# Optimization experiments

Measured on AMD Instinct MI355X. Metric: run time of the kernel, lower is better.

The kernel has to match this reference:

```python
import jax, jax.numpy as jnp
import numpy as np

B, S, D, H = 2, 4096, 512, 8
HD = D // H

def setup_inputs() -> dict:
    key = jax.random.key(0)
    ks = jax.random.split(key, 9)
    s = 1.0 / np.sqrt(D)
    inp = {"x": jax.random.normal(ks[0], (B, S, D), dtype=jnp.float32)}
    names = ["Wq", "Wk", "Wv", "Wo"]
    for i, n in enumerate(names):
        inp[n] = jax.random.uniform(ks[1 + 2 * i], (D, D), jnp.float32, -s, s)
        inp["b" + n[1]] = jax.random.uniform(ks[2 + 2 * i], (D,), jnp.float32, -s, s)
    return inp


def reference(x, Wq, bq, Wk, bk, Wv, bv, Wo, bo):
    # projections (torch Linear: x @ W.T + b)
    def proj(W, b):
        return (x @ W.T + b).reshape(B, S, H, HD).transpose(0, 2, 1, 3)  # [B,H,S,HD]
    q = proj(Wq, bq)
    k = proj(Wk, bk)
    v = proj(Wv, bv)
    scores = jnp.einsum("bhqd,bhkd->bhqk", q, k) / np.sqrt(HD).astype(np.float32)
    attn = jax.nn.softmax(scores, axis=-1)
    out = jnp.einsum("bhqk,bhkd->bhqd", attn, v)
    out = out.transpose(0, 2, 1, 3).reshape(B, S, D)
    return out @ Wo.T + bo
```

## Files before the change

kernel.cpp:

```cpp
#include <hip/hip_runtime.h>
#include <hip/hip_bf16.h>

#define DEV __device__ __forceinline__

typedef float f32x4 __attribute__((ext_vector_type(4)));
typedef float f32x16 __attribute__((ext_vector_type(16)));
typedef __bf16 bf16x8 __attribute__((ext_vector_type(8)));
typedef unsigned short u16;
typedef unsigned short u16x8 __attribute__((ext_vector_type(8)));

DEV u16 f2bf(float f) {
    __bf16 h = (__bf16)f;
    return __builtin_bit_cast(u16, h);
}
DEV float bf2f(u16 u) {
    __bf16 h = __builtin_bit_cast(__bf16, u);
    return (float)h;
}

DEV f32x4 mfma16(bf16x8 a, bf16x8 b, f32x4 c) {
    return __builtin_amdgcn_mfma_f32_16x16x32_bf16(a, b, c, 0, 0, 0);
}
DEV f32x16 mfma32(bf16x8 a, bf16x8 b, f32x16 c) {
    return __builtin_amdgcn_mfma_f32_32x32x16_bf16(a, b, c, 0, 0, 0);
}

DEV unsigned cvtpk(float lo, float hi) {
    unsigned r;
    asm("v_cvt_pk_bf16_f32 %0, %1, %2" : "=v"(r) : "v"(lo), "v"(hi));
    return r;
}
DEV void pswap(unsigned& a, unsigned& b) {
    asm volatile("v_permlane32_swap_b32 %0, %1" : "+v"(a), "+v"(b));
}

DEV int kidx(int row, int col) { return row * 64 + (col ^ ((row & 7) << 3)); }
DEV int xidx(int row, int col) { return row * 32 + (col ^ ((row & 3) << 3)); }

__global__ __launch_bounds__(256) void cvt_kernel(
    const float* __restrict__ wq, const float* __restrict__ wk,
    const float* __restrict__ wv, const float* __restrict__ wo,
    u16* __restrict__ wb)
{
    size_t e0 = ((size_t)blockIdx.x * 256 + threadIdx.x) * 8;
    int seg = (int)(e0 >> 18);
    const float* src = (seg == 0) ? wq : (seg == 1) ? wk : (seg == 2) ? wv : wo;
    u16* dst = wb + (size_t)seg * 262144;
    size_t off = e0 & 262143;
    f32x4 a = *(const f32x4*)(src + off);
    f32x4 b = *(const f32x4*)(src + off + 4);
    u16x8 o;
    #pragma unroll
    for (int i = 0; i < 4; ++i) { o[i] = f2bf(a[i]); o[i + 4] = f2bf(b[i]); }
    *(u16x8*)(dst + off) = o;
}

__global__ __launch_bounds__(256) void proj_qkv_kernel(
    const float* __restrict__ x, const u16* __restrict__ wb,
    const float* __restrict__ bq, const float* __restrict__ bk, const float* __restrict__ bv,
    u16* __restrict__ qo, u16* __restrict__ ko, u16* __restrict__ vo)
{
    __shared__ u16 Xs[128 * 32], Wsh[128 * 32];
    const int tid = threadIdx.x;
    const int m0 = blockIdx.x * 128, n0 = blockIdx.y * 128, z = blockIdx.z;
    const u16* W = wb + (size_t)z * 262144;
    const float* bias = (z == 0) ? bq : (z == 1) ? bk : bv;

    const int lane = tid & 63, wv = tid >> 6;
    const int g = lane >> 4, c = lane & 15;
    const int wr = wv >> 1, wcl = wv & 1;
    const int srow = tid >> 1, scol = (tid & 1) * 16;

    f32x4 acc[4][4] = {};

    for (int k0 = 0; k0 < 512; k0 += 32) {
        const float* xp = x + (size_t)(m0 + srow) * 512 + k0 + scol;
        const u16* wp = W + (size_t)(n0 + srow) * 512 + k0 + scol;
        f32x4 xa = *(const f32x4*)xp,       xb2 = *(const f32x4*)(xp + 4);
        f32x4 xc = *(const f32x4*)(xp + 8), xd  = *(const f32x4*)(xp + 12);
        uint4 wa = *(const uint4*)wp, wa2 = *(const uint4*)(wp + 8);
        __syncthreads();
        u16x8 px0, px1;
        #pragma unroll
        for (int j = 0; j < 4; ++j) {
            px0[j] = f2bf(xa[j]); px0[j + 4] = f2bf(xb2[j]);
            px1[j] = f2bf(xc[j]); px1[j + 4] = f2bf(xd[j]);
        }
        *(u16x8*)&Xs[xidx(srow, scol)]      = px0;
        *(u16x8*)&Xs[xidx(srow, scol + 8)]  = px1;
        *(uint4*)&Wsh[xidx(srow, scol)]     = wa;
        *(uint4*)&Wsh[xidx(srow, scol + 8)] = wa2;
        __syncthreads();

        bf16x8 af[4], bfr[4];
        #pragma unroll
        for (int mt = 0; mt < 4; ++mt)
            af[mt] = *(const bf16x8*)&Xs[xidx(wr * 64 + mt * 16 + c, g * 8)];
        #pragma unroll
        for (int nt = 0; nt < 4; ++nt)
            bfr[nt] = *(const bf16x8*)&Wsh[xidx(wcl * 64 + nt * 16 + c, g * 8)];

        if (z < 2) {
            #pragma unroll
            for (int mt = 0; mt < 4; ++mt)
                #pragma unroll
                for (int nt = 0; nt < 4; ++nt)
                    acc[mt][nt] = mfma16(af[mt], bfr[nt], acc[mt][nt]);
        } else {
            #pragma unroll
            for (int mt = 0; mt < 4; ++mt)
                #pragma unroll
                for (int nt = 0; nt < 4; ++nt)
                    acc[mt][nt] = mfma16(bfr[nt], af[mt], acc[mt][nt]);
        }
    }

    if (z < 2) {
        const float scale = (z == 0) ? 0.18033688011112042f : 1.0f;
        u16* outp = (z == 0) ? qo : ko;
        float bn[4];
        #pragma unroll
        for (int nt = 0; nt < 4; ++nt) bn[nt] = bias[n0 + wcl * 64 + nt * 16 + c];
        #pragma unroll
        for (int mt = 0; mt < 4; ++mt)
            #pragma unroll
            for (int r = 0; r < 4; ++r) {
                int mg = m0 + wr * 64 + mt * 16 + g * 4 + r;
                int b = mg >> 12, s = mg & 4095;
                #pragma unroll
                for (int nt = 0; nt < 4; ++nt) {
                    int ng = n0 + wcl * 64 + nt * 16 + c;
                    int h = ng >> 6, d = ng & 63;
                    outp[((size_t)(b * 8 + h) * 4096 + s) * 64 + d] =
                        f2bf((acc[mt][nt][r] + bn[nt]) * scale);
                }
            }
    } else {
        #pragma unroll
        for (int nt = 0; nt < 4; ++nt)
            #pragma unroll
            for (int r = 0; r < 4; ++r) {
                int ng = n0 + wcl * 64 + nt * 16 + g * 4 + r;
                int h = ng >> 6, d = ng & 63;
                float bnr = bias[ng];
                #pragma unroll
                for (int mt = 0; mt < 4; ++mt) {
                    int mg = m0 + wr * 64 + mt * 16 + c;
                    int b = mg >> 12, s = mg & 4095;
                    vo[((size_t)(b * 8 + h) * 64 + d) * 4096 + s] =
                        f2bf(acc[mt][nt][r] + bnr);
                }
            }
    }
}

__global__ __launch_bounds__(256, 4) void flash_attn_kernel(
    const u16* __restrict__ Q, const u16* __restrict__ K,
    const u16* __restrict__ Vt, u16* __restrict__ Opart, float* __restrict__ lbuf)
{
    __shared__ u16 Ks[2][64 * 64];
    __shared__ u16 Vs[2][64 * 64];

    const int tid = threadIdx.x;
    const int bh = blockIdx.y;
    const int q0 = blockIdx.x * 128;
    const int half = blockIdx.z;
    const int kvbase = half * 2048;
    const int lane = tid & 63, wv = tid >> 6;
    const int l31 = lane & 31, hi = lane >> 5;

    const u16* Qb = Q  + (size_t)bh * (4096 * 64);
    const u16* Kb = K  + (size_t)bh * (4096 * 64);
    const u16* Vb = Vt + (size_t)bh * (64 * 4096);

    const int qrow = q0 + wv * 32 + l31;
    bf16x8 qf[4];
    #pragma unroll
    for (int ds = 0; ds < 4; ++ds)
        qf[ds] = *(const bf16x8*)(Qb + (size_t)qrow * 64 + ds * 16 + hi * 8);

    f32x16 oA[2] = {};
    float l_ = 0.f;

    const int sr = tid >> 3, sc8 = (tid & 7) * 8;
    const u16* kp0 = Kb + (size_t)(kvbase + sr) * 64 + sc8;
    const u16* vp0 = Vb + (size_t)sr * 4096 + kvbase + sc8;

    uint4 rk0 = *(const uint4*)(kp0);
    uint4 rk1 = *(const uint4*)(kp0 + 32 * 64);
    uint4 rv0 = *(const uint4*)(vp0);
    uint4 rv1 = *(const uint4*)(vp0 + 32 * 4096);

    for (int t = 0; t < 32; ++t) {
        const int p = t & 1;
        *(uint4*)&Ks[p][kidx(sr, sc8)]      = rk0;
        *(uint4*)&Ks[p][kidx(sr + 32, sc8)] = rk1;
        *(uint4*)&Vs[p][kidx(sr, sc8)]      = rv0;
        *(uint4*)&Vs[p][kidx(sr + 32, sc8)] = rv1;
        if (t < 31) {
            const int kv1 = (t + 1) * 64;
            rk0 = *(const uint4*)(kp0 + (size_t)kv1 * 64);
            rk1 = *(const uint4*)(kp0 + (size_t)(kv1 + 32) * 64);
            rv0 = *(const uint4*)(vp0 + kv1);
            rv1 = *(const uint4*)(vp0 + 32 * 4096 + kv1);
        }
        __syncthreads();

        #pragma unroll
        for (int ct = 0; ct < 2; ++ct) {
            f32x16 sA = {};
            __builtin_amdgcn_s_setprio(1);
            #pragma unroll
            for (int ds = 0; ds < 4; ++ds) {
                bf16x8 kf = *(const bf16x8*)&Ks[p][kidx(ct * 32 + l31, ds * 16 + hi * 8)];
                sA = mfma32(kf, qf[ds], sA);
            }
            __builtin_amdgcn_s_setprio(0);

            float pv[16];
            #pragma unroll
            for (int r = 0; r < 16; ++r)
                pv[r] = __builtin_amdgcn_exp2f(sA[r]);
            #pragma unroll
            for (int r = 0; r < 16; r += 4)
                l_ += (pv[r] + pv[r + 1]) + (pv[r + 2] + pv[r + 3]);

            unsigned a0 = cvtpk(pv[0],  pv[1]),  a1 = cvtpk(pv[2],  pv[3]);
            unsigned b0 = cvtpk(pv[4],  pv[5]),  b1 = cvtpk(pv[6],  pv[7]);
            pswap(a0, b0); pswap(a1, b1);
            uint4 w0; w0.x = a0; w0.y = a1; w0.z = b0; w0.w = b1;
            bf16x8 pfa = __builtin_bit_cast(bf16x8, w0);
            unsigned c0 = cvtpk(pv[8],  pv[9]),  c1 = cvtpk(pv[10], pv[11]);
            unsigned d0 = cvtpk(pv[12], pv[13]), d1 = cvtpk(pv[14], pv[15]);
            pswap(c0, d0); pswap(c1, d1);
            uint4 w1; w1.x = c0; w1.y = c1; w1.z = d0; w1.w = d1;
            bf16x8 pfb = __builtin_bit_cast(bf16x8, w1);

            __builtin_amdgcn_s_setprio(1);
            #pragma unroll
            for (int hf = 0; hf < 2; ++hf) {
                const int ks = 2 * ct + hf;
                const bf16x8 pfx = hf ? pfb : pfa;
                bf16x8 vf0 = *(const bf16x8*)&Vs[p][kidx(l31,      ks * 16 + hi * 8)];
                bf16x8 vf1 = *(const bf16x8*)&Vs[p][kidx(32 + l31, ks * 16 + hi * 8)];
                oA[0] = mfma32(vf0, pfx, oA[0]);
                oA[1] = mfma32(vf1, pfx, oA[1]);
            }
            __builtin_amdgcn_s_setprio(0);
        }
    }

    float l_full = l_ + __shfl_xor(l_, 32);
    if (hi == 0)
        lbuf[(size_t)(half * 16 + bh) * 4096 + qrow] = l_full;

    const int b = bh >> 3, h = bh & 7;
    u16* Ob = Opart + (size_t)half * 4194304 +
              ((size_t)(b * 4096 + qrow)) * 512 + h * 64;
    #pragma unroll
    for (int dt = 0; dt < 2; ++dt) {
        const f32x16 oa = dt ? oA[1] : oA[0];
        #pragma unroll
        for (int qd = 0; qd < 4; ++qd) {
            unsigned w0 = cvtpk(oa[qd * 4 + 0], oa[qd * 4 + 1]);
            unsigned w1 = cvtpk(oa[qd * 4 + 2], oa[qd * 4 + 3]);
            uint2 st; st.x = w0; st.y = w1;
            *(uint2*)(Ob + dt * 32 + qd * 8 + hi * 4) = st;
        }
    }
}

__global__ __launch_bounds__(256) void combine_kernel(
    const u16* __restrict__ Opart, const float* __restrict__ lbuf,
    u16* __restrict__ obuf)
{
    const size_t idx8 = ((size_t)blockIdx.x * 256 + threadIdx.x) * 8;
    const int m = (int)(idx8 >> 9);
    const int hd = (int)(idx8 & 511);
    const int b = m >> 12, s = m & 4095, h = hd >> 6;
    const int bh = b * 8 + h;
    const float la = lbuf[(size_t)bh * 4096 + s];
    const float lb = lbuf[(size_t)(16 + bh) * 4096 + s];
    const float inv = 1.0f / (la + lb);
    u16x8 a = *(const u16x8*)(Opart + idx8);
    u16x8 c = *(const u16x8*)(Opart + 4194304 + idx8);
    u16x8 o;
    #pragma unroll
    for (int i = 0; i < 8; ++i)
        o[i] = f2bf((bf2f(a[i]) + bf2f(c[i])) * inv);
    *(u16x8*)(obuf + idx8) = o;
}

__global__ __launch_bounds__(256) void out_proj_kernel(
    const u16* __restrict__ Ob, const u16* __restrict__ Wob,
    const float* __restrict__ bo, float* __restrict__ out)
{
    __shared__ u16 Xs[128 * 32], Wsh[128 * 32];
    const int tid = threadIdx.x;
    const int m0 = blockIdx.x * 128, n0 = blockIdx.y * 128;

    const int lane = tid & 63, wv = tid >> 6;
    const int g = lane >> 4, c = lane & 15;
    const int wr = wv >> 1, wcl = wv & 1;
    const int srow = tid >> 1, scol = (tid & 1) * 16;

    f32x4 acc[4][4] = {};

    for (int k0 = 0; k0 < 512; k0 += 32) {
        const u16* xp = Ob  + (size_t)(m0 + srow) * 512 + k0 + scol;
        const u16* wp = Wob + (size_t)(n0 + srow) * 512 + k0 + scol;
        uint4 xa = *(const uint4*)xp, xa2 = *(const uint4*)(xp + 8);
        uint4 wa = *(const uint4*)wp, wa2 = *(const uint4*)(wp + 8);
        __syncthreads();
        *(uint4*)&Xs[xidx(srow, scol)]      = xa;
        *(uint4*)&Xs[xidx(srow, scol + 8)]  = xa2;
        *(uint4*)&Wsh[xidx(srow, scol)]     = wa;
        *(uint4*)&Wsh[xidx(srow, scol + 8)] = wa2;
        __syncthreads();

        bf16x8 af[4], bfr[4];
        #pragma unroll
        for (int mt = 0; mt < 4; ++mt)
            af[mt] = *(const bf16x8*)&Xs[xidx(wr * 64 + mt * 16 + c, g * 8)];
        #pragma unroll
        for (int nt = 0; nt < 4; ++nt)
            bfr[nt] = *(const bf16x8*)&Wsh[xidx(wcl * 64 + nt * 16 + c, g * 8)];

        #pragma unroll
        for (int mt = 0; mt < 4; ++mt)
            #pragma unroll
            for (int nt = 0; nt < 4; ++nt)
                acc[mt][nt] = mfma16(bfr[nt], af[mt], acc[mt][nt]);
    }

    #pragma unroll
    for (int nt = 0; nt < 4; ++nt) {
        f32x4 bi = *(const f32x4*)&bo[n0 + wcl * 64 + nt * 16 + g * 4];
        #pragma unroll
        for (int mt = 0; mt < 4; ++mt) {
            int m = m0 + wr * 64 + mt * 16 + c;
            f32x4 v;
            #pragma unroll
            for (int r = 0; r < 4; ++r) v[r] = acc[mt][nt][r] + bi[r];
            *(f32x4*)&out[(size_t)m * 512 + n0 + wcl * 64 + nt * 16 + g * 4] = v;
        }
    }
}

extern "C" void kernel_launch(void* const* d_in, const int* in_sizes, int n_in,
                              void* d_out, int out_size, void* d_ws, size_t ws_size,
                              hipStream_t stream) {
    const float* x  = (const float*)d_in[0];
    const float* Wq = (const float*)d_in[1];
    const float* bq = (const float*)d_in[2];
    const float* Wk = (const float*)d_in[3];
    const float* bk = (const float*)d_in[4];
    const float* Wv = (const float*)d_in[5];
    const float* bv = (const float*)d_in[6];
    const float* Wo = (const float*)d_in[7];
    const float* bo = (const float*)d_in[8];
    float* out = (float*)d_out;

    const size_t NQKV = (size_t)2 * 8 * 4096 * 64;
    u16* qw = (u16*)d_ws;
    u16* kw = qw + NQKV;
    u16* vw = kw + NQKV;
    u16* wbuf = vw + NQKV;
    float* lbuf = (float*)(wbuf + 4 * 262144);
    u16* opart = (u16*)d_out;
    u16* obuf = qw;

    cvt_kernel<<<512, 256, 0, stream>>>(Wq, Wk, Wv, Wo, wbuf);
    proj_qkv_kernel<<<dim3(64, 4, 3), 256, 0, stream>>>(x, wbuf, bq, bk, bv, qw, kw, vw);
    flash_attn_kernel<<<dim3(32, 16, 2), 256, 0, stream>>>(qw, kw, vw, opart, lbuf);
    combine_kernel<<<2048, 256, 0, stream>>>(opart, lbuf, obuf);
    out_proj_kernel<<<dim3(64, 4), 256, 0, stream>>>(obuf, wbuf + 3 * 262144, bo, out);
}
```

Measured before the change: 156.8 us.

## Pre-convert x to bf16 once and give each attention wave two query tiles

The conversion kernel now also converts x to bf16 into workspace. The QKV projection reads bf16 x directly instead of converting fp32 x in each of the 12 blocks that share a row tile (three projections times four column tiles). The flash-attention kernel now processes 64 query rows per wave (256 per block), reusing each K fragment and V fragment load across two query tiles. This halves the attention grid and lowers the occupancy bound from 4 to 2, trading fewer LDS reads and less K/V traffic for more registers and less parallelism.

```diff
diff --git a/kernel.cpp b/kernel.cpp
--- a/kernel.cpp
+++ b/kernel.cpp
@@ -38,15 +38,21 @@
 DEV int xidx(int row, int col) { return row * 32 + (col ^ ((row & 3) << 3)); }
 
 __global__ __launch_bounds__(256) void cvt_kernel(
-    const float* __restrict__ wq, const float* __restrict__ wk,
-    const float* __restrict__ wv, const float* __restrict__ wo,
-    u16* __restrict__ wb)
+    const float* __restrict__ x, const float* __restrict__ wq,
+    const float* __restrict__ wk, const float* __restrict__ wv,
+    const float* __restrict__ wo,
+    u16* __restrict__ xb, u16* __restrict__ wb)
 {
     size_t e0 = ((size_t)blockIdx.x * 256 + threadIdx.x) * 8;
-    int seg = (int)(e0 >> 18);
-    const float* src = (seg == 0) ? wq : (seg == 1) ? wk : (seg == 2) ? wv : wo;
-    u16* dst = wb + (size_t)seg * 262144;
-    size_t off = e0 & 262143;
+    const float* src; u16* dst; size_t off;
+    if (e0 < 4194304) { src = x; dst = xb; off = e0; }
+    else {
+        size_t r = e0 - 4194304;
+        int seg = (int)(r >> 18);
+        src = (seg == 0) ? wq : (seg == 1) ? wk : (seg == 2) ? wv : wo;
+        dst = wb + (size_t)seg * 262144;
+        off = r & 262143;
+    }
     f32x4 a = *(const f32x4*)(src + off);
     f32x4 b = *(const f32x4*)(src + off + 4);
     u16x8 o;
@@ -56,7 +62,7 @@
 }
 
 __global__ __launch_bounds__(256) void proj_qkv_kernel(
-    const float* __restrict__ x, const u16* __restrict__ wb,
+    const u16* __restrict__ xb, const u16* __restrict__ wb,
     const float* __restrict__ bq, const float* __restrict__ bk, const float* __restrict__ bv,
     u16* __restrict__ qo, u16* __restrict__ ko, u16* __restrict__ vo)
 {
@@ -74,20 +80,13 @@
     f32x4 acc[4][4] = {};
 
     for (int k0 = 0; k0 < 512; k0 += 32) {
-        const float* xp = x + (size_t)(m0 + srow) * 512 + k0 + scol;
-        const u16* wp = W + (size_t)(n0 + srow) * 512 + k0 + scol;
-        f32x4 xa = *(const f32x4*)xp,       xb2 = *(const f32x4*)(xp + 4);
-        f32x4 xc = *(const f32x4*)(xp + 8), xd  = *(const f32x4*)(xp + 12);
+        const u16* xp = xb + (size_t)(m0 + srow) * 512 + k0 + scol;
+        const u16* wp = W  + (size_t)(n0 + srow) * 512 + k0 + scol;
+        uint4 xa = *(const uint4*)xp, xa2 = *(const uint4*)(xp + 8);
         uint4 wa = *(const uint4*)wp, wa2 = *(const uint4*)(wp + 8);
         __syncthreads();
-        u16x8 px0, px1;
-        #pragma unroll
-        for (int j = 0; j < 4; ++j) {
-            px0[j] = f2bf(xa[j]); px0[j + 4] = f2bf(xb2[j]);
-            px1[j] = f2bf(xc[j]); px1[j + 4] = f2bf(xd[j]);
-        }
-        *(u16x8*)&Xs[xidx(srow, scol)]      = px0;
-        *(u16x8*)&Xs[xidx(srow, scol + 8)]  = px1;
+        *(uint4*)&Xs[xidx(srow, scol)]      = xa;
+        *(uint4*)&Xs[xidx(srow, scol + 8)]  = xa2;
         *(uint4*)&Wsh[xidx(srow, scol)]     = wa;
         *(uint4*)&Wsh[xidx(srow, scol + 8)] = wa2;
         __syncthreads();
@@ -154,7 +153,7 @@
     }
 }
 
-__global__ __launch_bounds__(256, 4) void flash_attn_kernel(
+__global__ __launch_bounds__(256, 2) void flash_attn_kernel(
     const u16* __restrict__ Q, const u16* __restrict__ K,
     const u16* __restrict__ Vt, u16* __restrict__ Opart, float* __restrict__ lbuf)
 {
@@ -163,7 +162,7 @@
 
     const int tid = threadIdx.x;
     const int bh = blockIdx.y;
-    const int q0 = blockIdx.x * 128;
+    const int q0 = blockIdx.x * 256;
     const int half = blockIdx.z;
     const int kvbase = half * 2048;
     const int lane = tid & 63, wv = tid >> 6;
@@ -173,14 +172,16 @@
     const u16* Kb = K  + (size_t)bh * (4096 * 64);
     const u16* Vb = Vt + (size_t)bh * (64 * 4096);
 
-    const int qrow = q0 + wv * 32 + l31;
-    bf16x8 qf[4];
-    #pragma unroll
-    for (int ds = 0; ds < 4; ++ds)
-        qf[ds] = *(const bf16x8*)(Qb + (size_t)qrow * 64 + ds * 16 + hi * 8);
-
-    f32x16 oA[2] = {};
-    float l_ = 0.f;
+    const int qbase = q0 + wv * 64;
+    bf16x8 qf[2][4];
+    #pragma unroll
+    for (int qt = 0; qt < 2; ++qt)
+        #pragma unroll
+        for (int ds = 0; ds < 4; ++ds)
+            qf[qt][ds] = *(const bf16x8*)(Qb + (size_t)(qbase + qt * 32 + l31) * 64 + ds * 16 + hi * 8);
+
+    f32x16 oA[2][2] = {};
+    float l_[2] = {0.f, 0.f};
 
     const int sr = tid >> 3, sc8 = (tid & 7) * 8;
     const u16* kp0 = Kb + (size_t)(kvbase + sr) * 64 + sc8;
@@ -208,64 +209,77 @@
 
         #pragma unroll
         for (int ct = 0; ct < 2; ++ct) {
-            f32x16 sA = {};
-            __builtin_amdgcn_s_setprio(1);
-            #pragma unroll
-            for (int ds = 0; ds < 4; ++ds) {
-                bf16x8 kf = *(const bf16x8*)&Ks[p][kidx(ct * 32 + l31, ds * 16 + hi * 8)];
-                sA = mfma32(kf, qf[ds], sA);
-            }
-            __builtin_amdgcn_s_setprio(0);
-
-            float pv[16];
-            #pragma unroll
-            for (int r = 0; r < 16; ++r)
-                pv[r] = __builtin_amdgcn_exp2f(sA[r]);
-            #pragma unroll
-            for (int r = 0; r < 16; r += 4)
-                l_ += (pv[r] + pv[r + 1]) + (pv[r + 2] + pv[r + 3]);
-
-            unsigned a0 = cvtpk(pv[0],  pv[1]),  a1 = cvtpk(pv[2],  pv[3]);
-            unsigned b0 = cvtpk(pv[4],  pv[5]),  b1 = cvtpk(pv[6],  pv[7]);
-            pswap(a0, b0); pswap(a1, b1);
-            uint4 w0; w0.x = a0; w0.y = a1; w0.z = b0; w0.w = b1;
-            bf16x8 pfa = __builtin_bit_cast(bf16x8, w0);
-            unsigned c0 = cvtpk(pv[8],  pv[9]),  c1 = cvtpk(pv[10], pv[11]);
-            unsigned d0 = cvtpk(pv[12], pv[13]), d1 = cvtpk(pv[14], pv[15]);
-            pswap(c0, d0); pswap(c1, d1);
-            uint4 w1; w1.x = c0; w1.y = c1; w1.z = d0; w1.w = d1;
-            bf16x8 pfb = __builtin_bit_cast(bf16x8, w1);
+            bf16x8 kf[4];
+            #pragma unroll
+            for (int ds = 0; ds < 4; ++ds)
+                kf[ds] = *(const bf16x8*)&Ks[p][kidx(ct * 32 + l31, ds * 16 + hi * 8)];
+
+            bf16x8 pf[2][2];
+            #pragma unroll
+            for (int qt = 0; qt < 2; ++qt) {
+                f32x16 sA = {};
+                __builtin_amdgcn_s_setprio(1);
+                #pragma unroll
+                for (int ds = 0; ds < 4; ++ds)
+                    sA = mfma32(kf[ds], qf[qt][ds], sA);
+                __builtin_amdgcn_s_setprio(0);
+
+                float pv[16];
+                #pragma unroll
+                for (int r = 0; r < 16; ++r)
+                    pv[r] = __builtin_amdgcn_exp2f(sA[r]);
+                #pragma unroll
+                for (int r = 0; r < 16; r += 4)
+                    l_[qt] += (pv[r] + pv[r + 1]) + (pv[r + 2] + pv[r + 3]);
+
+                unsigned a0 = cvtpk(pv[0],  pv[1]),  a1 = cvtpk(pv[2],  pv[3]);
+                unsigned b0 = cvtpk(pv[4],  pv[5]),  b1 = cvtpk(pv[6],  pv[7]);
+                pswap(a0, b0); pswap(a1, b1);
+                uint4 w0; w0.x = a0; w0.y = a1; w0.z = b0; w0.w = b1;
+                pf[qt][0] = __builtin_bit_cast(bf16x8, w0);
+                unsigned c0 = cvtpk(pv[8],  pv[9]),  c1 = cvtpk(pv[10], pv[11]);
+                unsigned d0 = cvtpk(pv[12], pv[13]), d1 = cvtpk(pv[14], pv[15]);
+                pswap(c0, d0); pswap(c1, d1);
+                uint4 w1; w1.x = c0; w1.y = c1; w1.z = d0; w1.w = d1;
+                pf[qt][1] = __builtin_bit_cast(bf16x8, w1);
+            }
 
             __builtin_amdgcn_s_setprio(1);
             #pragma unroll
             for (int hf = 0; hf < 2; ++hf) {
                 const int ks = 2 * ct + hf;
-                const bf16x8 pfx = hf ? pfb : pfa;
                 bf16x8 vf0 = *(const bf16x8*)&Vs[p][kidx(l31,      ks * 16 + hi * 8)];
                 bf16x8 vf1 = *(const bf16x8*)&Vs[p][kidx(32 + l31, ks * 16 + hi * 8)];
-                oA[0] = mfma32(vf0, pfx, oA[0]);
-                oA[1] = mfma32(vf1, pfx, oA[1]);
+                #pragma unroll
+                for (int qt = 0; qt < 2; ++qt) {
+                    oA[qt][0] = mfma32(vf0, pf[qt][hf], oA[qt][0]);
+                    oA[qt][1] = mfma32(vf1, pf[qt][hf], oA[qt][1]);
+                }
             }
             __builtin_amdgcn_s_setprio(0);
         }
     }
 
-    float l_full = l_ + __shfl_xor(l_, 32);
-    if (hi == 0)
-        lbuf[(size_t)(half * 16 + bh) * 4096 + qrow] = l_full;
-
     const int b = bh >> 3, h = bh & 7;
-    u16* Ob = Opart + (size_t)half * 4194304 +
-              ((size_t)(b * 4096 + qrow)) * 512 + h * 64;
-    #pragma unroll
-    for (int dt = 0; dt < 2; ++dt) {
-        const f32x16 oa = dt ? oA[1] : oA[0];
-        #pragma unroll
-        for (int qd = 0; qd < 4; ++qd) {
-            unsigned w0 = cvtpk(oa[qd * 4 + 0], oa[qd * 4 + 1]);
-            unsigned w1 = cvtpk(oa[qd * 4 + 2], oa[qd * 4 + 3]);
-            uint2 st; st.x = w0; st.y = w1;
-            *(uint2*)(Ob + dt * 32 + qd * 8 + hi * 4) = st;
+    #pragma unroll
+    for (int qt = 0; qt < 2; ++qt) {
+        const int qrow = qbase + qt * 32 + l31;
+        float l_full = l_[qt] + __shfl_xor(l_[qt], 32);
+        if (hi == 0)
+            lbuf[(size_t)(half * 16 + bh) * 4096 + qrow] = l_full;
+
+        u16* Ob = Opart + (size_t)half * 4194304 +
+                  ((size_t)(b * 4096 + qrow)) * 512 + h * 64;
+        #pragma unroll
+        for (int dt = 0; dt < 2; ++dt) {
+            const f32x16 oa = oA[qt][dt];
+            #pragma unroll
+            for (int qd = 0; qd < 4; ++qd) {
+                unsigned w0 = cvtpk(oa[qd * 4 + 0], oa[qd * 4 + 1]);
+                unsigned w1 = cvtpk(oa[qd * 4 + 2], oa[qd * 4 + 3]);
+                uint2 st; st.x = w0; st.y = w1;
+                *(uint2*)(Ob + dt * 32 + qd * 8 + hi * 4) = st;
+            }
         }
     }
 }
@@ -367,12 +381,13 @@
     u16* vw = kw + NQKV;
     u16* wbuf = vw + NQKV;
     float* lbuf = (float*)(wbuf + 4 * 262144);
+    u16* xbuf = (u16*)(lbuf + 2 * 16 * 4096);
     u16* opart = (u16*)d_out;
     u16* obuf = qw;
 
-    cvt_kernel<<<512, 256, 0, stream>>>(Wq, Wk, Wv, Wo, wbuf);
-    proj_qkv_kernel<<<dim3(64, 4, 3), 256, 0, stream>>>(x, wbuf, bq, bk, bv, qw, kw, vw);
-    flash_attn_kernel<<<dim3(32, 16, 2), 256, 0, stream>>>(qw, kw, vw, opart, lbuf);
+    cvt_kernel<<<2560, 256, 0, stream>>>(x, Wq, Wk, Wv, Wo, xbuf, wbuf);
+    proj_qkv_kernel<<<dim3(64, 4, 3), 256, 0, stream>>>(xbuf, wbuf, bq, bk, bv, qw, kw, vw);
+    flash_attn_kernel<<<dim3(16, 16, 2), 256, 0, stream>>>(qw, kw, vw, opart, lbuf);
     combine_kernel<<<2048, 256, 0, stream>>>(opart, lbuf, obuf);
     out_proj_kernel<<<dim3(64, 4), 256, 0, stream>>>(obuf, wbuf + 3 * 262144, bo, out);
 }
```

Measured after the change: 140.9 us. 10.1% less time.

## Pre-convert x to bf16 once and compute softmax row sums with MFMA

Applied to the files above, without the earlier changes.

The conversion kernel now also turns the fp32 input x into bf16 in workspace, so the QKV projection reads bf16 x directly instead of re-converting it in each of its 12 N/Z tile blocks. In the attention kernel, the per-lane scalar adds that built the softmax denominator are replaced by an MFMA of the bf16 probability fragments against an all-ones matrix. This moves VALU work onto the matrix cores but sums the rounded bf16 probabilities, which slightly changes the normaliser. The x path adds one extra pass over x in memory in exchange for halving what the projection reads.

```diff
diff --git a/kernel.cpp b/kernel.cpp
--- a/kernel.cpp
+++ b/kernel.cpp
@@ -38,15 +38,21 @@
 DEV int xidx(int row, int col) { return row * 32 + (col ^ ((row & 3) << 3)); }
 
 __global__ __launch_bounds__(256) void cvt_kernel(
-    const float* __restrict__ wq, const float* __restrict__ wk,
-    const float* __restrict__ wv, const float* __restrict__ wo,
-    u16* __restrict__ wb)
+    const float* __restrict__ x, const float* __restrict__ wq,
+    const float* __restrict__ wk, const float* __restrict__ wv,
+    const float* __restrict__ wo,
+    u16* __restrict__ xb, u16* __restrict__ wb)
 {
     size_t e0 = ((size_t)blockIdx.x * 256 + threadIdx.x) * 8;
-    int seg = (int)(e0 >> 18);
-    const float* src = (seg == 0) ? wq : (seg == 1) ? wk : (seg == 2) ? wv : wo;
-    u16* dst = wb + (size_t)seg * 262144;
-    size_t off = e0 & 262143;
+    const float* src; u16* dst; size_t off;
+    if (e0 < 4194304) { src = x; dst = xb; off = e0; }
+    else {
+        size_t r = e0 - 4194304;
+        int seg = (int)(r >> 18);
+        src = (seg == 0) ? wq : (seg == 1) ? wk : (seg == 2) ? wv : wo;
+        dst = wb + (size_t)seg * 262144;
+        off = r & 262143;
+    }
     f32x4 a = *(const f32x4*)(src + off);
     f32x4 b = *(const f32x4*)(src + off + 4);
     u16x8 o;
@@ -56,7 +62,7 @@
 }
 
 __global__ __launch_bounds__(256) void proj_qkv_kernel(
-    const float* __restrict__ x, const u16* __restrict__ wb,
+    const u16* __restrict__ xb, const u16* __restrict__ wb,
     const float* __restrict__ bq, const float* __restrict__ bk, const float* __restrict__ bv,
     u16* __restrict__ qo, u16* __restrict__ ko, u16* __restrict__ vo)
 {
@@ -74,20 +80,13 @@
     f32x4 acc[4][4] = {};
 
     for (int k0 = 0; k0 < 512; k0 += 32) {
-        const float* xp = x + (size_t)(m0 + srow) * 512 + k0 + scol;
-        const u16* wp = W + (size_t)(n0 + srow) * 512 + k0 + scol;
-        f32x4 xa = *(const f32x4*)xp,       xb2 = *(const f32x4*)(xp + 4);
-        f32x4 xc = *(const f32x4*)(xp + 8), xd  = *(const f32x4*)(xp + 12);
+        const u16* xp = xb + (size_t)(m0 + srow) * 512 + k0 + scol;
+        const u16* wp = W  + (size_t)(n0 + srow) * 512 + k0 + scol;
+        uint4 xa = *(const uint4*)xp, xa2 = *(const uint4*)(xp + 8);
         uint4 wa = *(const uint4*)wp, wa2 = *(const uint4*)(wp + 8);
         __syncthreads();
-        u16x8 px0, px1;
-        #pragma unroll
-        for (int j = 0; j < 4; ++j) {
-            px0[j] = f2bf(xa[j]); px0[j + 4] = f2bf(xb2[j]);
-            px1[j] = f2bf(xc[j]); px1[j + 4] = f2bf(xd[j]);
-        }
-        *(u16x8*)&Xs[xidx(srow, scol)]      = px0;
-        *(u16x8*)&Xs[xidx(srow, scol + 8)]  = px1;
+        *(uint4*)&Xs[xidx(srow, scol)]      = xa;
+        *(uint4*)&Xs[xidx(srow, scol + 8)]  = xa2;
         *(uint4*)&Wsh[xidx(srow, scol)]     = wa;
         *(uint4*)&Wsh[xidx(srow, scol + 8)] = wa2;
         __syncthreads();
@@ -173,6 +172,11 @@
     const u16* Kb = K  + (size_t)bh * (4096 * 64);
     const u16* Vb = Vt + (size_t)bh * (64 * 4096);
 
+    u16x8 onesu;
+    #pragma unroll
+    for (int i = 0; i < 8; ++i) onesu[i] = 0x3F80;
+    const bf16x8 ones = __builtin_bit_cast(bf16x8, onesu);
+
     const int qrow = q0 + wv * 32 + l31;
     bf16x8 qf[4];
     #pragma unroll
@@ -180,7 +184,7 @@
         qf[ds] = *(const bf16x8*)(Qb + (size_t)qrow * 64 + ds * 16 + hi * 8);
 
     f32x16 oA[2] = {};
-    float l_ = 0.f;
+    f32x16 oL = {};
 
     const int sr = tid >> 3, sc8 = (tid & 7) * 8;
     const u16* kp0 = Kb + (size_t)(kvbase + sr) * 64 + sc8;
@@ -221,9 +225,6 @@
             #pragma unroll
             for (int r = 0; r < 16; ++r)
                 pv[r] = __builtin_amdgcn_exp2f(sA[r]);
-            #pragma unroll
-            for (int r = 0; r < 16; r += 4)
-                l_ += (pv[r] + pv[r + 1]) + (pv[r + 2] + pv[r + 3]);
 
             unsigned a0 = cvtpk(pv[0],  pv[1]),  a1 = cvtpk(pv[2],  pv[3]);
             unsigned b0 = cvtpk(pv[4],  pv[5]),  b1 = cvtpk(pv[6],  pv[7]);
@@ -237,6 +238,8 @@
             bf16x8 pfb = __builtin_bit_cast(bf16x8, w1);
 
             __builtin_amdgcn_s_setprio(1);
+            oL = mfma32(ones, pfa, oL);
+            oL = mfma32(ones, pfb, oL);
             #pragma unroll
             for (int hf = 0; hf < 2; ++hf) {
                 const int ks = 2 * ct + hf;
@@ -250,9 +253,8 @@
         }
     }
 
-    float l_full = l_ + __shfl_xor(l_, 32);
     if (hi == 0)
-        lbuf[(size_t)(half * 16 + bh) * 4096 + qrow] = l_full;
+        lbuf[(size_t)(half * 16 + bh) * 4096 + qrow] = oL[0];
 
     const int b = bh >> 3, h = bh & 7;
     u16* Ob = Opart + (size_t)half * 4194304 +
@@ -367,11 +369,12 @@
     u16* vw = kw + NQKV;
     u16* wbuf = vw + NQKV;
     float* lbuf = (float*)(wbuf + 4 * 262144);
+    u16* xbuf = (u16*)(lbuf + 2 * 16 * 4096);
     u16* opart = (u16*)d_out;
     u16* obuf = qw;
 
-    cvt_kernel<<<512, 256, 0, stream>>>(Wq, Wk, Wv, Wo, wbuf);
-    proj_qkv_kernel<<<dim3(64, 4, 3), 256, 0, stream>>>(x, wbuf, bq, bk, bv, qw, kw, vw);
+    cvt_kernel<<<2560, 256, 0, stream>>>(x, Wq, Wk, Wv, Wo, xbuf, wbuf);
+    proj_qkv_kernel<<<dim3(64, 4, 3), 256, 0, stream>>>(xbuf, wbuf, bq, bk, bv, qw, kw, vw);
     flash_attn_kernel<<<dim3(32, 16, 2), 256, 0, stream>>>(qw, kw, vw, opart, lbuf);
     combine_kernel<<<2048, 256, 0, stream>>>(opart, lbuf, obuf);
     out_proj_kernel<<<dim3(64, 4), 256, 0, stream>>>(obuf, wbuf + 3 * 262144, bo, out);
```

After: 147.1 us. 6.2% less time.
